# Kernel optimization log

Measured on AMD Instinct MI355X. Metric: run time of the kernel, lower is better.

The kernel has to match this reference:

```python
import jax, jax.numpy as jnp
import numpy as np

B = 4096      # number of snakes (graphs)
L = 256       # fixed snake length (nodes per chain)
N = B * L     # total nodes
HID = 32
OUT = 32
AUX = 32
FIN = 64
N_FRUITS = 1
AUX_IN = 2 + 1 + N_FRUITS * 2  # = 5


def _chain_edges():
    # chain edges i<->i+1 within each graph, both directions (PyG undirected chain)
    base = np.arange(L - 1)
    src1 = (np.arange(B)[:, None] * L + base[None, :]).ravel()
    dst1 = src1 + 1
    src = np.concatenate([src1, dst1])
    dst = np.concatenate([dst1, src1])
    return np.stack([src, dst]).astype(np.int64)  # [2, 2*(L-1)*B]


def setup_inputs() -> dict:
    key = jax.random.key(0)
    ks = jax.random.split(key, 16)

    def lin(k, fan_in, fan_out):
        k1, k2 = jax.random.split(k)
        bound = 1.0 / np.sqrt(fan_in)
        W = jax.random.uniform(k1, (fan_in, fan_out), jnp.float32, -bound, bound)
        b = jax.random.uniform(k2, (fan_out,), jnp.float32, -bound, bound)
        return W, b

    x = jax.random.normal(ks[0], (N, 2), jnp.float32)
    heads = jax.random.normal(ks[1], (B, 2), jnp.float32)
    body_sizes = jax.random.uniform(ks[2], (B, 1), jnp.float32)
    fruits = jax.random.normal(ks[3], (B, N_FRUITS, 2), jnp.float32)

    W1, b1 = lin(ks[4], 2, HID)
    W2, b2 = lin(ks[5], HID, HID)
    Wr, br = lin(ks[6], HID, OUT)
    Wa1, ba1 = lin(ks[7], AUX_IN, AUX)
    Wa2, ba2 = lin(ks[8], AUX, AUX)
    Wc, bc = lin(ks[9], OUT + AUX, FIN)
    Wp, bp = lin(ks[10], FIN, 5)
    Wv, bv = lin(ks[11], FIN, 1)

    edge_index = jnp.asarray(_chain_edges())
    batch_ids = jnp.repeat(jnp.arange(B, dtype=jnp.int64), L)

    return dict(x=x, heads=heads, body_sizes=body_sizes, fruits=fruits,
                W1=W1, b1=b1, W2=W2, b2=b2, Wr=Wr, br=br,
                Wa1=Wa1, ba1=ba1, Wa2=Wa2, ba2=ba2, Wc=Wc, bc=bc,
                Wp=Wp, bp=bp, Wv=Wv, bv=bv,
                edge_index=edge_index, batch_ids=batch_ids)


def _gcn_conv(h, W, b, src, dst):
    # PyG GCNConv: out = D^{-1/2} (A + I) D^{-1/2} (h W) + b, deg counts self-loop
    h = h @ W  # [N, F]
    ones = jnp.ones(src.shape[0], h.dtype)
    deg = jax.ops.segment_sum(ones, dst, num_segments=N) + 1.0  # self-loop
    dinv = jax.lax.rsqrt(deg)
    norm = dinv[src] * dinv[dst]  # [E]
    agg = jax.ops.segment_sum(norm[:, None] * h[src], dst, num_segments=N)
    agg = agg + (dinv * dinv)[:, None] * h  # self-loop messages
    return agg + b


def reference(x, heads, body_sizes, fruits,
              W1, b1, W2, b2, Wr, br, Wa1, ba1, Wa2, ba2,
              Wc, bc, Wp, bp, Wv, bv, edge_index, batch_ids):
    src, dst = edge_index[0], edge_index[1]
    h = jax.nn.relu(_gcn_conv(x, W1, b1, src, dst))
    h = jax.nn.relu(_gcn_conv(h, W2, b2, src, dst))
    # global mean pool per graph
    pooled = jax.ops.segment_sum(h, batch_ids, num_segments=B)
    counts = jax.ops.segment_sum(jnp.ones(N, h.dtype), batch_ids, num_segments=B)
    pooled = pooled / counts[:, None]
    body_emb = pooled @ Wr + br  # [B, OUT]

    aux_input = jnp.concatenate([heads, body_sizes,
                                 fruits.reshape(fruits.shape[0], -1)], axis=-1)
    aux = jax.nn.relu(aux_input @ Wa1 + ba1)
    aux = jax.nn.relu(aux @ Wa2 + ba2)

    combined = jnp.concatenate([body_emb, aux], axis=-1)
    combined = jax.nn.relu(combined @ Wc + bc)
    logits = combined @ Wp + bp  # [B, 5]
    value = combined @ Wv + bv   # [B, 1]
    return logits, value
```

## Files before the change

### kernel.cpp

```cpp
#include <hip/hip_runtime.h>
#include <hip/hip_bf16.h>


#define NB  4096
#define CL  256
#define HID 32
#define FIN 64

typedef __attribute__((ext_vector_type(8))) short    bf16x8;
typedef __attribute__((ext_vector_type(4))) float    f32x4;
typedef __attribute__((ext_vector_type(4))) unsigned u32x4;

__device__ __forceinline__ unsigned pkbf(float a, float b) {
    __hip_bfloat162 hb = __float22bfloat162_rn(make_float2(a, b));
    unsigned u; __builtin_memcpy(&u, &hb, sizeof(u));
    return u;
}
__device__ __forceinline__ float bflo(unsigned u) { return __builtin_bit_cast(float, u << 16); }
__device__ __forceinline__ float bfhi(unsigned u) { return __builtin_bit_cast(float, u & 0xffff0000u); }

__device__ __forceinline__ void gcn_coef(int n, float& nc, float& nl, float& nr) {
    const float IS3 = 0.57735026918962576f, IS2 = 0.70710678118654752f;
    const float dn = (n == 0 || n == CL - 1) ? IS2 : IS3;
    nc = dn * dn;
    nl = (n > 0)      ? dn * ((n == 1)      ? IS2 : IS3) : 0.0f;
    nr = (n < CL - 1) ? dn * ((n == CL - 2) ? IS2 : IS3) : 0.0f;
}

__global__ __launch_bounds__(256, 4) void snake_fused(
    const float* __restrict__ x,
    const float* __restrict__ heads,
    const float* __restrict__ body_sizes,
    const float* __restrict__ fruits,
    const float* __restrict__ W1, const float* __restrict__ b1,
    const float* __restrict__ W2, const float* __restrict__ b2,
    const float* __restrict__ Wr, const float* __restrict__ br,
    const float* __restrict__ Wa1, const float* __restrict__ ba1,
    const float* __restrict__ Wa2, const float* __restrict__ ba2,
    const float* __restrict__ Wc, const float* __restrict__ bc,
    const float* __restrict__ Wp, const float* __restrict__ bp,
    const float* __restrict__ Wv, const float* __restrict__ bv,
    float* __restrict__ out)
{
    __shared__ __align__(16) float wsc[4][FIN];

    const int tid  = threadIdx.x;
    const int w    = tid >> 6;
    const int lane = tid & 63;
    const int g    = lane >> 4;
    const int c    = lane & 15;
    const int gs   = blockIdx.x * 4 + w;

    bf16x8 Bh[2], Bl[2];
    #pragma unroll
    for (int nt = 0; nt < 2; ++nt) {
        unsigned hh[4], ll[4];
        #pragma unroll
        for (int p = 0; p < 4; ++p) {
            const float wa = W2[(8 * g + 2 * p)     * HID + c + 16 * nt];
            const float wb = W2[(8 * g + 2 * p + 1) * HID + c + 16 * nt];
            const unsigned hu = pkbf(wa, wb);
            hh[p] = hu;
            ll[p] = pkbf(wa - bflo(hu), wb - bfhi(hu));
        }
        u32x4 H = {hh[0], hh[1], hh[2], hh[3]};
        u32x4 L = {ll[0], ll[1], ll[2], ll[3]};
        Bh[nt] = __builtin_bit_cast(bf16x8, H);
        Bl[nt] = __builtin_bit_cast(bf16x8, L);
    }
    const float b2v0 = b2[c], b2v1 = b2[c + 16];

    const float4 W1a0 = *(const float4*)(W1 + 8 * g);
    const float4 W1a1 = *(const float4*)(W1 + 8 * g + 4);
    const float4 W1b0 = *(const float4*)(W1 + HID + 8 * g);
    const float4 W1b1 = *(const float4*)(W1 + HID + 8 * g + 4);
    const float4 b1v0 = *(const float4*)(b1 + 8 * g);
    const float4 b1v1 = *(const float4*)(b1 + 8 * g + 4);

    const float THIRD = 0.33333333333333333f;
    const float I23   = 0.40824829046386302f;

    const float2* xs = (const float2*)x + gs * CL;

    auto compute_tile = [&](int t, f32x4* accT) {
        const int m = 16 * t + c;
        const float2 xcv = xs[m];
        const float2 xlv = xs[m - (m > 0)];
        const float2 xrv = xs[m + (m < CL - 1)];
        float ncd, nld, nrd;
        if (t == 0 || t == 15) { gcn_coef(m, ncd, nld, nrd); }
        else { ncd = THIRD; nld = THIRD; nrd = THIRD; }
        const float sa = ncd * xcv.x + nld * xlv.x + nrd * xrv.x;
        const float sb = ncd * xcv.y + nld * xlv.y + nrd * xrv.y;
        const float r0 = fmaxf(fmaf(sa, W1a0.x, fmaf(sb, W1b0.x, b1v0.x)), 0.f);
        const float r1 = fmaxf(fmaf(sa, W1a0.y, fmaf(sb, W1b0.y, b1v0.y)), 0.f);
        const float r2 = fmaxf(fmaf(sa, W1a0.z, fmaf(sb, W1b0.z, b1v0.z)), 0.f);
        const float r3 = fmaxf(fmaf(sa, W1a0.w, fmaf(sb, W1b0.w, b1v0.w)), 0.f);
        const float r4 = fmaxf(fmaf(sa, W1a1.x, fmaf(sb, W1b1.x, b1v1.x)), 0.f);
        const float r5 = fmaxf(fmaf(sa, W1a1.y, fmaf(sb, W1b1.y, b1v1.y)), 0.f);
        const float r6 = fmaxf(fmaf(sa, W1a1.z, fmaf(sb, W1b1.z, b1v1.z)), 0.f);
        const float r7 = fmaxf(fmaf(sa, W1a1.w, fmaf(sb, W1b1.w, b1v1.w)), 0.f);
        const unsigned h0 = pkbf(r0, r1), h1 = pkbf(r2, r3);
        const unsigned h2 = pkbf(r4, r5), h3 = pkbf(r6, r7);
        const unsigned q0 = pkbf(r0 - bflo(h0), r1 - bfhi(h0));
        const unsigned q1 = pkbf(r2 - bflo(h1), r3 - bfhi(h1));
        const unsigned q2 = pkbf(r4 - bflo(h2), r5 - bfhi(h2));
        const unsigned q3 = pkbf(r6 - bflo(h3), r7 - bfhi(h3));
        u32x4 HU = {h0, h1, h2, h3};
        u32x4 LU = {q0, q1, q2, q3};
        const bf16x8 ah = __builtin_bit_cast(bf16x8, HU);
        const bf16x8 al = __builtin_bit_cast(bf16x8, LU);
        #pragma unroll
        for (int nt = 0; nt < 2; ++nt) {
            f32x4 a0 = {0.f, 0.f, 0.f, 0.f};
            a0 = __builtin_amdgcn_mfma_f32_16x16x32_bf16(ah, Bh[nt], a0, 0, 0, 0);
            a0 = __builtin_amdgcn_mfma_f32_16x16x32_bf16(al, Bh[nt], a0, 0, 0, 0);
            a0 = __builtin_amdgcn_mfma_f32_16x16x32_bf16(ah, Bl[nt], a0, 0, 0, 0);
            accT[nt] = a0;
        }
    };

    f32x4 accP[2], accC[2], accN[2];
    { f32x4 z = {0.f, 0.f, 0.f, 0.f}; accP[0] = z; accP[1] = z; accN[0] = z; accN[1] = z; }
    compute_tile(0, accC);
    float sum0 = 0.f, sum1 = 0.f;

    #pragma unroll
    for (int t = 0; t < 16; ++t) {
        if (t < 15) compute_tile(t + 1, accN);
        const bool fL = (t == 0)  && (g == 0);
        const bool fR = (t == 15) && (g == 3);
        const float c0  = fL ? 0.5f : THIRD;
        const float r0c = fL ? I23  : THIRD;
        const float l1c = fL ? I23  : THIRD;
        const float c3  = fR ? 0.5f : THIRD;
        const float l3c = fR ? I23  : THIRD;
        const float r2c = fR ? I23  : THIRD;
        #pragma unroll
        for (int nt = 0; nt < 2; ++nt) {
            const f32x4 v = accC[nt];
            const float Lsend = (g == 3) ? accP[nt][3] : v[3];
            const int   Lsrc  = (g == 0) ? (c + 48) : (lane - 16);
            float L = __shfl(Lsend, Lsrc, 64);
            if (t == 0)  L = (g == 0) ? 0.f : L;
            const float Rsend = (g == 0) ? accN[nt][0] : v[0];
            const int   Rsrc  = (g == 3) ? c : (lane + 16);
            float R = __shfl(Rsend, Rsrc, 64);
            if (t == 15) R = (g == 3) ? 0.f : R;
            const float bb = nt ? b2v1 : b2v0;
            const float h0 = fmaxf(fmaf(c0,    v[0], fmaf(THIRD, L,    fmaf(r0c,   v[1], bb))), 0.f);
            const float h1 = fmaxf(fmaf(THIRD, v[1], fmaf(l1c,   v[0], fmaf(THIRD, v[2], bb))), 0.f);
            const float h2 = fmaxf(fmaf(THIRD, v[2], fmaf(THIRD, v[1], fmaf(r2c,   v[3], bb))), 0.f);
            const float h3 = fmaxf(fmaf(c3,    v[3], fmaf(l3c,   v[2], fmaf(THIRD, R,    bb))), 0.f);
            const float hs = (h0 + h1) + (h2 + h3);
            if (nt == 0) sum0 += hs; else sum1 += hs;
        }
        accP[0] = accC[0]; accP[1] = accC[1];
        accC[0] = accN[0]; accC[1] = accN[1];
    }

    sum0 += __shfl_xor(sum0, 16, 64); sum0 += __shfl_xor(sum0, 32, 64);
    sum1 += __shfl_xor(sum1, 16, 64); sum1 += __shfl_xor(sum1, 32, 64);
    wsc[w][c]      = sum0 * (1.0f / CL);
    wsc[w][c + 16] = sum1 * (1.0f / CL);

    if (lane >= 32) {
        const int cc = lane - 32;
        float a = ba1[cc];
        a = fmaf(heads[2 * gs],      Wa1[0 * HID + cc], a);
        a = fmaf(heads[2 * gs + 1],  Wa1[1 * HID + cc], a);
        a = fmaf(body_sizes[gs],     Wa1[2 * HID + cc], a);
        a = fmaf(fruits[2 * gs],     Wa1[3 * HID + cc], a);
        a = fmaf(fruits[2 * gs + 1], Wa1[4 * HID + cc], a);
        wsc[w][32 + cc] = fmaxf(a, 0.f);
    }
    {
        const int  hh = lane >> 5;
        const int  cc = lane & 31;
        const float* Wsel = hh ? Wa2 : Wr;
        const float  bsel = hh ? ba2[cc] : br[cc];
        const float* lsel = &wsc[w][32 * hh];
        float cv = bsel;
        #pragma unroll
        for (int k4 = 0; k4 < 8; ++k4) {
            const f32x4 p = *(const f32x4*)&lsel[4 * k4];
            cv = fmaf(p[0], Wsel[(4 * k4 + 0) * HID + cc], cv);
            cv = fmaf(p[1], Wsel[(4 * k4 + 1) * HID + cc], cv);
            cv = fmaf(p[2], Wsel[(4 * k4 + 2) * HID + cc], cv);
            cv = fmaf(p[3], Wsel[(4 * k4 + 3) * HID + cc], cv);
        }
        cv = hh ? fmaxf(cv, 0.f) : cv;
        wsc[w][lane] = cv;
    }
    {
        float cb = bc[lane];
        #pragma unroll
        for (int k4 = 0; k4 < 16; ++k4) {
            const f32x4 p = *(const f32x4*)&wsc[w][4 * k4];
            cb = fmaf(p[0], Wc[(4 * k4 + 0) * FIN + lane], cb);
            cb = fmaf(p[1], Wc[(4 * k4 + 1) * FIN + lane], cb);
            cb = fmaf(p[2], Wc[(4 * k4 + 2) * FIN + lane], cb);
            cb = fmaf(p[3], Wc[(4 * k4 + 3) * FIN + lane], cb);
        }
        cb = fmaxf(cb, 0.f);
        float s0 = cb * Wp[lane * 5 + 0];
        float s1 = cb * Wp[lane * 5 + 1];
        float s2 = cb * Wp[lane * 5 + 2];
        float s3 = cb * Wp[lane * 5 + 3];
        float s4 = cb * Wp[lane * 5 + 4];
        float s5 = cb * Wv[lane];
        #pragma unroll
        for (int m = 1; m <= 32; m <<= 1) {
            s0 += __shfl_xor(s0, m, 64);
            s1 += __shfl_xor(s1, m, 64);
            s2 += __shfl_xor(s2, m, 64);
            s3 += __shfl_xor(s3, m, 64);
            s4 += __shfl_xor(s4, m, 64);
            s5 += __shfl_xor(s5, m, 64);
        }
        if (lane == 0) {
            out[gs * 5 + 0] = s0 + bp[0];
            out[gs * 5 + 1] = s1 + bp[1];
            out[gs * 5 + 2] = s2 + bp[2];
            out[gs * 5 + 3] = s3 + bp[3];
            out[gs * 5 + 4] = s4 + bp[4];
            out[NB * 5 + gs] = s5 + bv[0];
        }
    }
}

extern "C" void kernel_launch(void* const* d_in, const int* in_sizes, int n_in,
                              void* d_out, int out_size, void* d_ws, size_t ws_size,
                              hipStream_t stream) {
    const float* x          = (const float*)d_in[0];
    const float* heads      = (const float*)d_in[1];
    const float* body_sizes = (const float*)d_in[2];
    const float* fruits     = (const float*)d_in[3];
    const float* W1 = (const float*)d_in[4];
    const float* b1 = (const float*)d_in[5];
    const float* W2 = (const float*)d_in[6];
    const float* b2 = (const float*)d_in[7];
    const float* Wr = (const float*)d_in[8];
    const float* br = (const float*)d_in[9];
    const float* Wa1 = (const float*)d_in[10];
    const float* ba1 = (const float*)d_in[11];
    const float* Wa2 = (const float*)d_in[12];
    const float* ba2 = (const float*)d_in[13];
    const float* Wc = (const float*)d_in[14];
    const float* bc = (const float*)d_in[15];
    const float* Wp = (const float*)d_in[16];
    const float* bp = (const float*)d_in[17];
    const float* Wv = (const float*)d_in[18];
    const float* bv = (const float*)d_in[19];

    float* out = (float*)d_out;
    snake_fused<<<NB / 4, 256, 0, stream>>>(
        x, heads, body_sizes, fruits,
        W1, b1, W2, b2, Wr, br, Wa1, ba1, Wa2, ba2,
        Wc, bc, Wp, bp, Wv, bv, out);
}
```

Baseline: 128.5 us.

## Aggregate layer-2 neighbours before the W2 matmul to drop cross-lane shuffles

Uses linearity to move the second GCN aggregation ahead of the W2 MFMA. Each lane recomputes the layer-1 ReLU outputs for its left, centre and right neighbours from five x values, sums them with the normalisation weights, and then multiplies by W2 pre-scaled by one third. This removes the post-MFMA neighbour shuffles and the previous/current/next accumulator pipelining. In exchange each lane does roughly three times the layer-1 ALU work and issues more x loads, using packed two-wide float math to keep that cost down.

```diff
diff --git a/kernel.cpp b/kernel.cpp
--- a/kernel.cpp
+++ b/kernel.cpp
@@ -9,6 +9,7 @@
 
 typedef __attribute__((ext_vector_type(8))) short    bf16x8;
 typedef __attribute__((ext_vector_type(4))) float    f32x4;
+typedef __attribute__((ext_vector_type(2))) float    f32x2;
 typedef __attribute__((ext_vector_type(4))) unsigned u32x4;
 
 __device__ __forceinline__ unsigned pkbf(float a, float b) {
@@ -18,6 +19,16 @@
 }
 __device__ __forceinline__ float bflo(unsigned u) { return __builtin_bit_cast(float, u << 16); }
 __device__ __forceinline__ float bfhi(unsigned u) { return __builtin_bit_cast(float, u & 0xffff0000u); }
+
+__device__ __forceinline__ f32x2 sfma(float s, f32x2 v, f32x2 a) {
+    f32x2 sv = {s, s};
+    return __builtin_elementwise_fma(sv, v, a);
+}
+__device__ __forceinline__ f32x2 smul(float s, f32x2 v) { f32x2 sv = {s, s}; return sv * v; }
+__device__ __forceinline__ f32x2 vmax0(f32x2 v) {
+    f32x2 z = {0.f, 0.f};
+    return __builtin_elementwise_max(v, z);
+}
 
 __device__ __forceinline__ void gcn_coef(int n, float& nc, float& nl, float& nr) {
     const float IS3 = 0.57735026918962576f, IS2 = 0.70710678118654752f;
@@ -51,14 +62,16 @@
     const int c    = lane & 15;
     const int gs   = blockIdx.x * 4 + w;
 
+    const float THIRD = 0.33333333333333333f;
+
     bf16x8 Bh[2], Bl[2];
     #pragma unroll
     for (int nt = 0; nt < 2; ++nt) {
         unsigned hh[4], ll[4];
         #pragma unroll
         for (int p = 0; p < 4; ++p) {
-            const float wa = W2[(8 * g + 2 * p)     * HID + c + 16 * nt];
-            const float wb = W2[(8 * g + 2 * p + 1) * HID + c + 16 * nt];
+            const float wa = W2[(8 * g + 2 * p)     * HID + c + 16 * nt] * THIRD;
+            const float wb = W2[(8 * g + 2 * p + 1) * HID + c + 16 * nt] * THIRD;
             const unsigned hu = pkbf(wa, wb);
             hh[p] = hu;
             ll[p] = pkbf(wa - bflo(hu), wb - bfhi(hu));
@@ -76,87 +89,86 @@
     const float4 W1b1 = *(const float4*)(W1 + HID + 8 * g + 4);
     const float4 b1v0 = *(const float4*)(b1 + 8 * g);
     const float4 b1v1 = *(const float4*)(b1 + 8 * g + 4);
-
-    const float THIRD = 0.33333333333333333f;
-    const float I23   = 0.40824829046386302f;
+    const f32x2 W1ap[4] = {{W1a0.x, W1a0.y}, {W1a0.z, W1a0.w}, {W1a1.x, W1a1.y}, {W1a1.z, W1a1.w}};
+    const f32x2 W1bp[4] = {{W1b0.x, W1b0.y}, {W1b0.z, W1b0.w}, {W1b1.x, W1b1.y}, {W1b1.z, W1b1.w}};
+    const f32x2 b1p[4]  = {{b1v0.x, b1v0.y}, {b1v0.z, b1v0.w}, {b1v1.x, b1v1.y}, {b1v1.z, b1v1.w}};
 
     const float2* xs = (const float2*)x + gs * CL;
 
-    auto compute_tile = [&](int t, f32x4* accT) {
+    float sum0 = 0.f, sum1 = 0.f;
+
+    auto r1p = [&](const f32x2 Sx, int p) -> f32x2 {
+        return vmax0(sfma(Sx.x, W1ap[p], sfma(Sx.y, W1bp[p], b1p[p])));
+    };
+
+    #pragma unroll
+    for (int t = 0; t < 16; ++t) {
         const int m = 16 * t + c;
-        const float2 xcv = xs[m];
-        const float2 xlv = xs[m - (m > 0)];
-        const float2 xrv = xs[m + (m < CL - 1)];
-        float ncd, nld, nrd;
-        if (t == 0 || t == 15) { gcn_coef(m, ncd, nld, nrd); }
-        else { ncd = THIRD; nld = THIRD; nrd = THIRD; }
-        const float sa = ncd * xcv.x + nld * xlv.x + nrd * xrv.x;
-        const float sb = ncd * xcv.y + nld * xlv.y + nrd * xrv.y;
-        const float r0 = fmaxf(fmaf(sa, W1a0.x, fmaf(sb, W1b0.x, b1v0.x)), 0.f);
-        const float r1 = fmaxf(fmaf(sa, W1a0.y, fmaf(sb, W1b0.y, b1v0.y)), 0.f);
-        const float r2 = fmaxf(fmaf(sa, W1a0.z, fmaf(sb, W1b0.z, b1v0.z)), 0.f);
-        const float r3 = fmaxf(fmaf(sa, W1a0.w, fmaf(sb, W1b0.w, b1v0.w)), 0.f);
-        const float r4 = fmaxf(fmaf(sa, W1a1.x, fmaf(sb, W1b1.x, b1v1.x)), 0.f);
-        const float r5 = fmaxf(fmaf(sa, W1a1.y, fmaf(sb, W1b1.y, b1v1.y)), 0.f);
-        const float r6 = fmaxf(fmaf(sa, W1a1.z, fmaf(sb, W1b1.z, b1v1.z)), 0.f);
-        const float r7 = fmaxf(fmaf(sa, W1a1.w, fmaf(sb, W1b1.w, b1v1.w)), 0.f);
-        const unsigned h0 = pkbf(r0, r1), h1 = pkbf(r2, r3);
-        const unsigned h2 = pkbf(r4, r5), h3 = pkbf(r6, r7);
-        const unsigned q0 = pkbf(r0 - bflo(h0), r1 - bfhi(h0));
-        const unsigned q1 = pkbf(r2 - bflo(h1), r3 - bfhi(h1));
-        const unsigned q2 = pkbf(r4 - bflo(h2), r5 - bfhi(h2));
-        const unsigned q3 = pkbf(r6 - bflo(h3), r7 - bfhi(h3));
-        u32x4 HU = {h0, h1, h2, h3};
-        u32x4 LU = {q0, q1, q2, q3};
+        int im2 = m - 2, im1 = m - 1, ip1 = m + 1, ip2 = m + 2;
+        if (t == 0)  { im2 = im2 < 0 ? 0 : im2;  im1 = im1 < 0 ? 0 : im1; }
+        if (t == 15) { ip1 = ip1 > CL - 1 ? CL - 1 : ip1;  ip2 = ip2 > CL - 1 ? CL - 1 : ip2; }
+        const float2 v0 = xs[im2], v1 = xs[im1], v2 = xs[m], v3 = xs[ip1], v4 = xs[ip2];
+        const f32x2 x0 = {v0.x, v0.y}, x1 = {v1.x, v1.y}, x2 = {v2.x, v2.y};
+        const f32x2 x3 = {v3.x, v3.y}, x4 = {v4.x, v4.y};
+
+        f32x2 SxL, SxC, SxR;
+        if (t == 0 || t == 15) {
+            float aC, aL, aR;
+            gcn_coef(im1, aC, aL, aR);
+            SxL = sfma(aC, x1, sfma(aL, x0, smul(aR, x2)));
+            gcn_coef(m, aC, aL, aR);
+            SxC = sfma(aC, x2, sfma(aL, x1, smul(aR, x3)));
+            gcn_coef(ip1, aC, aL, aR);
+            SxR = sfma(aC, x3, sfma(aL, x2, smul(aR, x4)));
+        } else {
+            SxL = smul(THIRD, (x0 + x1) + x2);
+            SxC = smul(THIRD, (x1 + x2) + x3);
+            SxR = smul(THIRD, (x2 + x3) + x4);
+        }
+
+        float cC2 = 1.f, cL2 = 1.f, cR2 = 1.f;
+        if (t == 0 || t == 15) {
+            gcn_coef(m, cC2, cL2, cR2);
+            cC2 *= 3.f; cL2 *= 3.f; cR2 *= 3.f;
+        }
+
+        unsigned HH[4], LL[4];
+        #pragma unroll
+        for (int p = 0; p < 4; ++p) {
+            const f32x2 rL = r1p(SxL, p);
+            const f32x2 rC = r1p(SxC, p);
+            const f32x2 rR = r1p(SxR, p);
+            f32x2 Sh;
+            if (t == 0 || t == 15)
+                Sh = sfma(cL2, rL, sfma(cC2, rC, smul(cR2, rR)));
+            else
+                Sh = (rL + rC) + rR;
+            const unsigned h = pkbf(Sh.x, Sh.y);
+            const f32x2 hf = {bflo(h), bfhi(h)};
+            const f32x2 lo = Sh - hf;
+            HH[p] = h;
+            LL[p] = pkbf(lo.x, lo.y);
+        }
+        u32x4 HU = {HH[0], HH[1], HH[2], HH[3]};
+        u32x4 LU = {LL[0], LL[1], LL[2], LL[3]};
         const bf16x8 ah = __builtin_bit_cast(bf16x8, HU);
         const bf16x8 al = __builtin_bit_cast(bf16x8, LU);
+
         #pragma unroll
         for (int nt = 0; nt < 2; ++nt) {
             f32x4 a0 = {0.f, 0.f, 0.f, 0.f};
             a0 = __builtin_amdgcn_mfma_f32_16x16x32_bf16(ah, Bh[nt], a0, 0, 0, 0);
             a0 = __builtin_amdgcn_mfma_f32_16x16x32_bf16(al, Bh[nt], a0, 0, 0, 0);
             a0 = __builtin_amdgcn_mfma_f32_16x16x32_bf16(ah, Bl[nt], a0, 0, 0, 0);
-            accT[nt] = a0;
-        }
-    };
-
-    f32x4 accP[2], accC[2], accN[2];
-    { f32x4 z = {0.f, 0.f, 0.f, 0.f}; accP[0] = z; accP[1] = z; accN[0] = z; accN[1] = z; }
-    compute_tile(0, accC);
-    float sum0 = 0.f, sum1 = 0.f;
-
-    #pragma unroll
-    for (int t = 0; t < 16; ++t) {
-        if (t < 15) compute_tile(t + 1, accN);
-        const bool fL = (t == 0)  && (g == 0);
-        const bool fR = (t == 15) && (g == 3);
-        const float c0  = fL ? 0.5f : THIRD;
-        const float r0c = fL ? I23  : THIRD;
-        const float l1c = fL ? I23  : THIRD;
-        const float c3  = fR ? 0.5f : THIRD;
-        const float l3c = fR ? I23  : THIRD;
-        const float r2c = fR ? I23  : THIRD;
-        #pragma unroll
-        for (int nt = 0; nt < 2; ++nt) {
-            const f32x4 v = accC[nt];
-            const float Lsend = (g == 3) ? accP[nt][3] : v[3];
-            const int   Lsrc  = (g == 0) ? (c + 48) : (lane - 16);
-            float L = __shfl(Lsend, Lsrc, 64);
-            if (t == 0)  L = (g == 0) ? 0.f : L;
-            const float Rsend = (g == 0) ? accN[nt][0] : v[0];
-            const int   Rsrc  = (g == 3) ? c : (lane + 16);
-            float R = __shfl(Rsend, Rsrc, 64);
-            if (t == 15) R = (g == 3) ? 0.f : R;
             const float bb = nt ? b2v1 : b2v0;
-            const float h0 = fmaxf(fmaf(c0,    v[0], fmaf(THIRD, L,    fmaf(r0c,   v[1], bb))), 0.f);
-            const float h1 = fmaxf(fmaf(THIRD, v[1], fmaf(l1c,   v[0], fmaf(THIRD, v[2], bb))), 0.f);
-            const float h2 = fmaxf(fmaf(THIRD, v[2], fmaf(THIRD, v[1], fmaf(r2c,   v[3], bb))), 0.f);
-            const float h3 = fmaxf(fmaf(c3,    v[3], fmaf(l3c,   v[2], fmaf(THIRD, R,    bb))), 0.f);
-            const float hs = (h0 + h1) + (h2 + h3);
+            const f32x2 bv2 = {bb, bb};
+            f32x2 q01 = {a0[0], a0[1]}, q23 = {a0[2], a0[3]};
+            q01 = vmax0(q01 + bv2);
+            q23 = vmax0(q23 + bv2);
+            const f32x2 qs = q01 + q23;
+            const float hs = qs.x + qs.y;
             if (nt == 0) sum0 += hs; else sum1 += hs;
         }
-        accP[0] = accC[0]; accP[1] = accC[1];
-        accC[0] = accN[0]; accC[1] = accN[1];
     }
 
     sum0 += __shfl_xor(sum0, 16, 64); sum0 += __shfl_xor(sum0, 32, 64);
```

Result: slower. 133.1 us (+3.6%).
